# Optimization experiments

Measured on AMD Instinct MI355X. Metric: run time of the kernel, lower is better.

The kernel has to match this reference:

```python
import jax, jax.numpy as jnp
import numpy as np

TEMPERATURE = 0.07
EPS = 1e-8  # torch CosineSimilarity eps


def setup_inputs() -> dict:
    key = jax.random.key(0)
    k1, k2, k3 = jax.random.split(key, 3)
    N, D = 8192, 512
    features = jax.random.normal(k1, (N, D), dtype=jnp.float32)
    positive_mask = jax.random.randint(k2, (N, N), 0, 2, dtype=jnp.int32)
    negative_mask = jax.random.randint(k3, (N, N), 0, 2, dtype=jnp.int32)
    return {"features": features, "positive_mask": positive_mask, "negative_mask": negative_mask}


def reference(features, positive_mask, negative_mask):
    N = positive_mask.shape[0]
    self_contrast = 1.0 - jnp.eye(N, dtype=features.dtype)  # zero diagonal
    pos = positive_mask.astype(features.dtype) * self_contrast  # [N, N]
    neg = negative_mask.astype(features.dtype) * self_contrast  # [N, N]

    # cosine similarity via normalized matmul (same math as broadcasted CosineSimilarity)
    norm = jnp.maximum(jnp.linalg.norm(features, axis=1, keepdims=True), EPS)
    fn = features / norm  # [N, D]
    sim = jnp.matmul(fn, fn.T) / TEMPERATURE  # [N, N]

    logits_max = jax.lax.stop_gradient(jnp.max(sim, axis=1, keepdims=True))
    e = jnp.exp(sim - logits_max)  # [N, N]

    positives = e * pos
    log_neg_sum = jnp.log(jnp.sum(e * neg, axis=1, keepdims=True))  # [N, 1]
    log_prob = positives - log_neg_sum  # [N, N] (faithful to source: exp-masked, not log)

    cardinal = jnp.sum(pos, axis=1)
    cardinal = jnp.where(cardinal == 0, 1.0, cardinal)
    log_prob_sum = jnp.sum(log_prob * pos, axis=1)
    loss = -log_prob_sum / cardinal
    return jnp.mean(loss)
```

## Files before the change

kernel.cpp:

```cpp
#include <hip/hip_runtime.h>
#include <hip/hip_bf16.h>
#include <math.h>

#define NN 8192
#define DD 512
#define INV_T 14.285714285714286f
#define NWPR 128

typedef __attribute__((ext_vector_type(8))) short s16x8;
typedef __attribute__((ext_vector_type(4))) float f32x4;

__device__ __forceinline__ unsigned short f32_to_bf16(float f) {
  unsigned int u = __float_as_uint(f);
  u += 0x7FFFu + ((u >> 16) & 1u);
  return (unsigned short)(u >> 16);
}

__device__ __forceinline__ void async16(const void* g, void* l) {
  __builtin_amdgcn_global_load_lds((__attribute__((address_space(1))) void*)(void*)g,
                                   (__attribute__((address_space(3))) void*)l,
                                   16, 0, 0);
}

__global__ __launch_bounds__(256) void normalize_kernel(const float* __restrict__ f,
                                                        unsigned short* __restrict__ fnb) {
  const int wave = threadIdx.x >> 6;
  const int lane = threadIdx.x & 63;
  const int row  = blockIdx.x * 4 + wave;
  const float* src = f + (size_t)row * DD + lane * 8;
  float4 v0 = *(const float4*)src;
  float4 v1 = *(const float4*)(src + 4);
  float ss = v0.x*v0.x + v0.y*v0.y + v0.z*v0.z + v0.w*v0.w
           + v1.x*v1.x + v1.y*v1.y + v1.z*v1.z + v1.w*v1.w;
  #pragma unroll
  for (int o = 32; o; o >>= 1) ss += __shfl_xor(ss, o);
  const float r = 1.0f / fmaxf(sqrtf(ss), 1e-8f);
  ushort4 a, b;
  a.x = f32_to_bf16(v0.x * r); a.y = f32_to_bf16(v0.y * r);
  a.z = f32_to_bf16(v0.z * r); a.w = f32_to_bf16(v0.w * r);
  b.x = f32_to_bf16(v1.x * r); b.y = f32_to_bf16(v1.y * r);
  b.z = f32_to_bf16(v1.z * r); b.w = f32_to_bf16(v1.w * r);
  unsigned short* dst = fnb + (size_t)row * DD + lane * 8;
  *(ushort4*)dst = a;
  *(ushort4*)(dst + 4) = b;
}

__global__ __launch_bounds__(256) void pack_kernel(const int* __restrict__ posm,
                                                   const int* __restrict__ negm,
                                                   unsigned long long* __restrict__ pb,
                                                   unsigned long long* __restrict__ nb) {
  const int lane = threadIdx.x & 63;
  const long long gw = (long long)((blockIdx.x * 256 + threadIdx.x) >> 6);
  const long long nwaves = (long long)((gridDim.x * 256) >> 6);
  const long long NW = (long long)NN * NN / 64;
  for (long long w0 = gw * 8; w0 < NW; w0 += nwaves * 8) {
    unsigned long long bp[8], bn[8];
    #pragma unroll
    for (int u = 0; u < 8; ++u) {
      const size_t idx = (size_t)(w0 + u) * 64 + lane;
      const int p = __builtin_nontemporal_load(posm + idx);
      const int n = __builtin_nontemporal_load(negm + idx);
      bp[u] = __ballot(p != 0);
      bn[u] = __ballot(n != 0);
    }
    if (lane == 0) {
      #pragma unroll
      for (int u = 0; u < 8; u += 2) {
        ulonglong2 vp; vp.x = bp[u]; vp.y = bp[u + 1];
        ulonglong2 vn; vn.x = bn[u]; vn.y = bn[u + 1];
        *(ulonglong2*)(pb + w0 + u) = vp;
        *(ulonglong2*)(nb + w0 + u) = vn;
      }
    }
  }
}

__global__ __launch_bounds__(256) void fused_kernel(const unsigned short* __restrict__ fnb,
                                                    const unsigned long long* __restrict__ pb,
                                                    const unsigned long long* __restrict__ nb,
                                                    float* __restrict__ Spos,
                                                    float* __restrict__ Sneg,
                                                    float* __restrict__ Pcnt) {
  const int bid = blockIdx.x;
  int bi = (int)(64.5 - sqrt(64.5 * 64.5 - 2.0 * (double)bid));
  while (64 * bi - bi * (bi - 1) / 2 > bid) --bi;
  while (64 * (bi + 1) - (bi + 1) * bi / 2 <= bid) ++bi;
  const int bj = bi + (bid - (64 * bi - bi * (bi - 1) / 2));
  const int I = bi * 128;
  const int J = bj * 128;

  const int tid  = threadIdx.x;
  const int wave = tid >> 6;
  const int lane = tid & 63;
  const int wm = wave >> 1;
  const int wn = wave & 1;
  const int q   = lane >> 4;
  const int c16 = lane & 15;

  __shared__ alignas(16) unsigned short lA[128 * 32];
  __shared__ alignas(16) unsigned short lB[128 * 32];

  f32x4 acc[4][4];
  const f32x4 z4 = {0.f, 0.f, 0.f, 0.f};
  #pragma unroll
  for (int mt = 0; mt < 4; ++mt)
    #pragma unroll
    for (int nt = 0; nt < 4; ++nt) acc[mt][nt] = z4;

  for (int kk = 0; kk < DD / 32; ++kk) {
    const int k0 = kk * 32;
    #pragma unroll
    for (int c = 0; c < 2; ++c) {
      const int fidx = tid + c * 256;
      const int row  = fidx >> 2;
      const int p    = fidx & 3;
      const int csrc = (p ^ ((row >> 1) & 3)) & 3;
      async16(fnb + (size_t)(I + row) * DD + k0 + csrc * 8, (char*)lA + fidx * 16);
      async16(fnb + (size_t)(J + row) * DD + k0 + csrc * 8, (char*)lB + fidx * 16);
    }
    __syncthreads();

    s16x8 aF[4], bF[4];
    #pragma unroll
    for (int t = 0; t < 4; ++t) {
      const int arow = wm * 64 + t * 16 + c16;
      const int apos = (q ^ ((arow >> 1) & 3)) & 3;
      aF[t] = *(const s16x8*)((const char*)lA + arow * 64 + apos * 16);
      const int brow = wn * 64 + t * 16 + c16;
      const int bpos = (q ^ ((brow >> 1) & 3)) & 3;
      bF[t] = *(const s16x8*)((const char*)lB + brow * 64 + bpos * 16);
    }
    #pragma unroll
    for (int mt = 0; mt < 4; ++mt)
      #pragma unroll
      for (int nt = 0; nt < 4; ++nt)
        acc[mt][nt] = __builtin_amdgcn_mfma_f32_16x16x32_bf16(aF[mt], bF[nt], acc[mt][nt], 0, 0, 0);
    __syncthreads();
  }

  const bool offdiag = (bi != bj);
  const bool hasdiag = (bi == bj) && (wm == wn);
  const int jw = bj * 2 + wn;

  unsigned long long pT[4], nT[4];
  if (offdiag) {
    #pragma unroll
    for (int nt = 0; nt < 4; ++nt) {
      const int col = J + wn * 64 + nt * 16 + c16;
      const size_t tw = (size_t)col * NWPR + bi * 2 + wm;
      pT[nt] = pb[tw];
      nT[nt] = nb[tw];
    }
  }
  float tsp[4] = {0,0,0,0}, tsn[4] = {0,0,0,0};

  #pragma unroll
  for (int mt = 0; mt < 4; ++mt) {
    const int rbase = I + wm * 64 + mt * 16 + q * 4;
    unsigned long long pw[4], nw[4];
    #pragma unroll
    for (int r = 0; r < 4; ++r) {
      const size_t w = (size_t)(rbase + r) * NWPR + jw;
      pw[r] = pb[w];
      nw[r] = nb[w];
      if (hasdiag) {
        const unsigned long long m = ~(1ULL << (mt * 16 + q * 4 + r));
        pw[r] &= m;
        nw[r] &= m;
      }
    }
    float dsp[4] = {0,0,0,0}, dsn[4] = {0,0,0,0};
    #pragma unroll
    for (int nt = 0; nt < 4; ++nt) {
      float e[4];
      #pragma unroll
      for (int r = 0; r < 4; ++r)
        e[r] = __expf(acc[mt][nt][r] * INV_T - INV_T);
      const int bpos = nt * 16 + c16;
      #pragma unroll
      for (int r = 0; r < 4; ++r) {
        const float pf = (float)((pw[r] >> bpos) & 1ULL);
        const float nf = (float)((nw[r] >> bpos) & 1ULL);
        dsp[r] = fmaf(e[r], pf, dsp[r]);
        dsn[r] = fmaf(e[r], nf, dsn[r]);
      }
      if (offdiag) {
        const int bt = mt * 16 + q * 4;
        #pragma unroll
        for (int r = 0; r < 4; ++r) {
          tsp[nt] = fmaf(e[r], (float)((pT[nt] >> (bt + r)) & 1ULL), tsp[nt]);
          tsn[nt] = fmaf(e[r], (float)((nT[nt] >> (bt + r)) & 1ULL), tsn[nt]);
        }
      }
    }
    #pragma unroll
    for (int r = 0; r < 4; ++r) {
      float a = dsp[r], b = dsn[r];
      #pragma unroll
      for (int o = 1; o <= 8; o <<= 1) {
        a += __shfl_xor(a, o);
        b += __shfl_xor(b, o);
      }
      if (c16 == 0) {
        atomicAdd(&Spos[rbase + r], a);
        atomicAdd(&Sneg[rbase + r], b);
        atomicAdd(&Pcnt[rbase + r], (float)__popcll(pw[r]));
      }
    }
  }

  if (offdiag) {
    #pragma unroll
    for (int nt = 0; nt < 4; ++nt) {
      float a = tsp[nt], b = tsn[nt];
      a += __shfl_xor(a, 16); a += __shfl_xor(a, 32);
      b += __shfl_xor(b, 16); b += __shfl_xor(b, 32);
      if (q == 0) {
        const int col = J + wn * 64 + nt * 16 + c16;
        atomicAdd(&Spos[col], a);
        atomicAdd(&Sneg[col], b);
        atomicAdd(&Pcnt[col], (float)__popcll(pT[nt]));
      }
    }
  }
}

__global__ __launch_bounds__(256) void finalize_kernel(const float* __restrict__ Spos,
                                                       const float* __restrict__ Sneg,
                                                       const float* __restrict__ Pcnt,
                                                       float* __restrict__ out) {
  float local = 0.f;
  for (int i = threadIdx.x; i < NN; i += 256) {
    const float sp = Spos[i], sn = Sneg[i], pc = Pcnt[i];
    const float card = (pc == 0.f) ? 1.f : pc;
    local += (logf(sn) * pc - sp) / card;
  }
  #pragma unroll
  for (int o = 32; o; o >>= 1) local += __shfl_xor(local, o);
  __shared__ float red[4];
  if ((threadIdx.x & 63) == 0) red[threadIdx.x >> 6] = local;
  __syncthreads();
  if (threadIdx.x == 0)
    out[0] = (red[0] + red[1] + red[2] + red[3]) * (1.0f / (float)NN);
}

extern "C" void kernel_launch(void* const* d_in, const int* in_sizes, int n_in,
                              void* d_out, int out_size, void* d_ws, size_t ws_size,
                              hipStream_t stream) {
  const float* feat = (const float*)d_in[0];
  const int* posm   = (const int*)d_in[1];
  const int* negm   = (const int*)d_in[2];
  float* out = (float*)d_out;

  char* ws = (char*)d_ws;
  unsigned short* fnb = (unsigned short*)ws;
  unsigned long long* pbit = (unsigned long long*)(ws + (size_t)8 * 1024 * 1024);
  unsigned long long* nbit = (unsigned long long*)(ws + (size_t)16 * 1024 * 1024);
  float* Spos = (float*)(ws + (size_t)24 * 1024 * 1024);
  float* Sneg = Spos + NN;
  float* Pcnt = Sneg + NN;

  hipMemsetAsync(Spos, 0, 3 * NN * sizeof(float), stream);
  normalize_kernel<<<NN / 4, 256, 0, stream>>>(feat, fnb);
  pack_kernel<<<4096, 256, 0, stream>>>(posm, negm, pbit, nbit);
  fused_kernel<<<2080, 256, 0, stream>>>(fnb, pbit, nbit, Spos, Sneg, Pcnt);
  finalize_kernel<<<1, 256, 0, stream>>>(Spos, Sneg, Pcnt, out);
}
```

Measured before the change: 669.6 us.

## Fuse mask bit-packing into the fused GEMM kernel via LDS bitmasks

Removes the separate pack_kernel that turned the int32 masks into global bitmaps. Each block of the triangular GEMM now loads its own 128x128 tile of both masks, plus the transposed tile for off-diagonal blocks, ballots them into LDS bitmasks, and reads those in the epilogue. This avoids writing and re-reading the packed bitmaps and one kernel launch. The int32 mask traffic (512 MB total) is still read once. It now happens inside the GEMM kernel before the k-loop, which may serialize memory latency with compute unless occupancy hides it.

```diff
diff --git a/kernel.cpp b/kernel.cpp
--- a/kernel.cpp
+++ b/kernel.cpp
@@ -5,7 +5,6 @@
 #define NN 8192
 #define DD 512
 #define INV_T 14.285714285714286f
-#define NWPR 128
 
 typedef __attribute__((ext_vector_type(8))) short s16x8;
 typedef __attribute__((ext_vector_type(4))) float f32x4;
@@ -45,39 +44,9 @@
   *(ushort4*)(dst + 4) = b;
 }
 
-__global__ __launch_bounds__(256) void pack_kernel(const int* __restrict__ posm,
-                                                   const int* __restrict__ negm,
-                                                   unsigned long long* __restrict__ pb,
-                                                   unsigned long long* __restrict__ nb) {
-  const int lane = threadIdx.x & 63;
-  const long long gw = (long long)((blockIdx.x * 256 + threadIdx.x) >> 6);
-  const long long nwaves = (long long)((gridDim.x * 256) >> 6);
-  const long long NW = (long long)NN * NN / 64;
-  for (long long w0 = gw * 8; w0 < NW; w0 += nwaves * 8) {
-    unsigned long long bp[8], bn[8];
-    #pragma unroll
-    for (int u = 0; u < 8; ++u) {
-      const size_t idx = (size_t)(w0 + u) * 64 + lane;
-      const int p = __builtin_nontemporal_load(posm + idx);
-      const int n = __builtin_nontemporal_load(negm + idx);
-      bp[u] = __ballot(p != 0);
-      bn[u] = __ballot(n != 0);
-    }
-    if (lane == 0) {
-      #pragma unroll
-      for (int u = 0; u < 8; u += 2) {
-        ulonglong2 vp; vp.x = bp[u]; vp.y = bp[u + 1];
-        ulonglong2 vn; vn.x = bn[u]; vn.y = bn[u + 1];
-        *(ulonglong2*)(pb + w0 + u) = vp;
-        *(ulonglong2*)(nb + w0 + u) = vn;
-      }
-    }
-  }
-}
-
 __global__ __launch_bounds__(256) void fused_kernel(const unsigned short* __restrict__ fnb,
-                                                    const unsigned long long* __restrict__ pb,
-                                                    const unsigned long long* __restrict__ nb,
+                                                    const int* __restrict__ posm,
+                                                    const int* __restrict__ negm,
                                                     float* __restrict__ Spos,
                                                     float* __restrict__ Sneg,
                                                     float* __restrict__ Pcnt) {
@@ -88,6 +57,7 @@
   const int bj = bi + (bid - (64 * bi - bi * (bi - 1) / 2));
   const int I = bi * 128;
   const int J = bj * 128;
+  const bool offdiag = (bi != bj);
 
   const int tid  = threadIdx.x;
   const int wave = tid >> 6;
@@ -99,6 +69,36 @@
 
   __shared__ alignas(16) unsigned short lA[128 * 32];
   __shared__ alignas(16) unsigned short lB[128 * 32];
+  __shared__ alignas(16) unsigned long long mdir[2][128][2];
+  __shared__ alignas(16) unsigned long long mtr [2][128][2];
+
+  {
+    const int tile = wave >> 1;
+    const int msel = wave & 1;
+    const int R0 = tile ? J : I;
+    const int C0 = tile ? I : J;
+    const int* mb = msel ? negm : posm;
+    unsigned long long (*dst)[2] = tile ? mtr[msel] : mdir[msel];
+    if (!(tile && !offdiag)) {
+      for (int k = 0; k < 128; k += 8) {
+        int v[16];
+        #pragma unroll
+        for (int u = 0; u < 16; ++u)
+          v[u] = __builtin_nontemporal_load(
+              mb + (size_t)(R0 + k + (u >> 1)) * NN + C0 + (u & 1) * 64 + lane);
+        unsigned long long b[16];
+        #pragma unroll
+        for (int u = 0; u < 16; ++u) b[u] = __ballot(v[u] != 0);
+        if (lane == 0) {
+          #pragma unroll
+          for (int u = 0; u < 16; u += 2) {
+            ulonglong2 t; t.x = b[u]; t.y = b[u + 1];
+            *(ulonglong2*)&dst[k + (u >> 1)][0] = t;
+          }
+        }
+      }
+    }
+  }
 
   f32x4 acc[4][4];
   const f32x4 z4 = {0.f, 0.f, 0.f, 0.f};
@@ -138,31 +138,28 @@
     __syncthreads();
   }
 
-  const bool offdiag = (bi != bj);
   const bool hasdiag = (bi == bj) && (wm == wn);
-  const int jw = bj * 2 + wn;
 
   unsigned long long pT[4], nT[4];
   if (offdiag) {
     #pragma unroll
     for (int nt = 0; nt < 4; ++nt) {
-      const int col = J + wn * 64 + nt * 16 + c16;
-      const size_t tw = (size_t)col * NWPR + bi * 2 + wm;
-      pT[nt] = pb[tw];
-      nT[nt] = nb[tw];
+      const int cl = wn * 64 + nt * 16 + c16;
+      pT[nt] = mtr[0][cl][wm];
+      nT[nt] = mtr[1][cl][wm];
     }
   }
   float tsp[4] = {0,0,0,0}, tsn[4] = {0,0,0,0};
 
   #pragma unroll
   for (int mt = 0; mt < 4; ++mt) {
-    const int rbase = I + wm * 64 + mt * 16 + q * 4;
+    const int rl = wm * 64 + mt * 16 + q * 4;
+    const int rbase = I + rl;
     unsigned long long pw[4], nw[4];
     #pragma unroll
     for (int r = 0; r < 4; ++r) {
-      const size_t w = (size_t)(rbase + r) * NWPR + jw;
-      pw[r] = pb[w];
-      nw[r] = nb[w];
+      pw[r] = mdir[0][rl + r][wn];
+      nw[r] = mdir[1][rl + r][wn];
       if (hasdiag) {
         const unsigned long long m = ~(1ULL << (mt * 16 + q * 4 + r));
         pw[r] &= m;
@@ -254,15 +251,12 @@
 
   char* ws = (char*)d_ws;
   unsigned short* fnb = (unsigned short*)ws;
-  unsigned long long* pbit = (unsigned long long*)(ws + (size_t)8 * 1024 * 1024);
-  unsigned long long* nbit = (unsigned long long*)(ws + (size_t)16 * 1024 * 1024);
-  float* Spos = (float*)(ws + (size_t)24 * 1024 * 1024);
+  float* Spos = (float*)(ws + (size_t)8 * 1024 * 1024);
   float* Sneg = Spos + NN;
   float* Pcnt = Sneg + NN;
 
   hipMemsetAsync(Spos, 0, 3 * NN * sizeof(float), stream);
   normalize_kernel<<<NN / 4, 256, 0, stream>>>(feat, fnb);
-  pack_kernel<<<4096, 256, 0, stream>>>(posm, negm, pbit, nbit);
-  fused_kernel<<<2080, 256, 0, stream>>>(fnb, pbit, nbit, Spos, Sneg, Pcnt);
+  fused_kernel<<<2080, 256, 0, stream>>>(fnb, posm, negm, Spos, Sneg, Pcnt);
   finalize_kernel<<<1, 256, 0, stream>>>(Spos, Sneg, Pcnt, out);
 }
```

New measurement: 654.4 us. -2.3%, faster.

## Vectorize mask packing with prefetch and reduce tile partials in shared memory

Applied to the files above, without the earlier changes.

The pack kernel now loads 16-byte vectors per lane with a double-buffered prefetch across 8 iterations. It writes the bitmasks in a permuted bit order that matches the MFMA accumulator layout, so the fused kernel extracts bits with simpler shifts. The fused kernel applies exp to all accumulators up front and reduces row and column partial sums in shared memory before issuing one set of global atomics per tile, which cuts global atomic traffic. It also sets a launch bound of 3 blocks per SM. The bit-order permutation must stay consistent between producer and consumer, and the new occupancy bound risks register pressure.

```diff
diff --git a/kernel.cpp b/kernel.cpp
--- a/kernel.cpp
+++ b/kernel.cpp
@@ -5,10 +5,10 @@
 #define NN 8192
 #define DD 512
 #define INV_T 14.285714285714286f
-#define NWPR 128
 
 typedef __attribute__((ext_vector_type(8))) short s16x8;
 typedef __attribute__((ext_vector_type(4))) float f32x4;
+typedef __attribute__((ext_vector_type(4))) int   i32x4;
 
 __device__ __forceinline__ unsigned short f32_to_bf16(float f) {
   unsigned int u = __float_as_uint(f);
@@ -50,37 +50,68 @@
                                                    unsigned long long* __restrict__ pb,
                                                    unsigned long long* __restrict__ nb) {
   const int lane = threadIdx.x & 63;
-  const long long gw = (long long)((blockIdx.x * 256 + threadIdx.x) >> 6);
-  const long long nwaves = (long long)((gridDim.x * 256) >> 6);
-  const long long NW = (long long)NN * NN / 64;
-  for (long long w0 = gw * 8; w0 < NW; w0 += nwaves * 8) {
-    unsigned long long bp[8], bn[8];
-    #pragma unroll
-    for (int u = 0; u < 8; ++u) {
-      const size_t idx = (size_t)(w0 + u) * 64 + lane;
-      const int p = __builtin_nontemporal_load(posm + idx);
-      const int n = __builtin_nontemporal_load(negm + idx);
-      bp[u] = __ballot(p != 0);
-      bn[u] = __ballot(n != 0);
-    }
-    if (lane == 0) {
-      #pragma unroll
-      for (int u = 0; u < 8; u += 2) {
-        ulonglong2 vp; vp.x = bp[u]; vp.y = bp[u + 1];
-        ulonglong2 vn; vn.x = bn[u]; vn.y = bn[u + 1];
-        *(ulonglong2*)(pb + w0 + u) = vp;
-        *(ulonglong2*)(nb + w0 + u) = vn;
-      }
-    }
-  }
-}
-
-__global__ __launch_bounds__(256) void fused_kernel(const unsigned short* __restrict__ fnb,
-                                                    const unsigned long long* __restrict__ pb,
-                                                    const unsigned long long* __restrict__ nb,
-                                                    float* __restrict__ Spos,
-                                                    float* __restrict__ Sneg,
-                                                    float* __restrict__ Pcnt) {
+  const int gw = (int)((blockIdx.x * 256 + threadIdx.x) >> 6);
+  const int lofs = lane * 4;
+
+  i32x4 vp[2][4], vn[2][4];
+  #pragma unroll
+  for (int u = 0; u < 4; ++u) {
+    const size_t b = ((size_t)gw * 4 + u) * 256 + lofs;
+    vp[0][u] = __builtin_nontemporal_load((const i32x4*)(posm + b));
+    vn[0][u] = __builtin_nontemporal_load((const i32x4*)(negm + b));
+  }
+  #pragma unroll 1
+  for (int it = 0; it < 8; ++it) {
+    const int cur = it & 1, nxt = cur ^ 1;
+    if (it < 7) {
+      #pragma unroll
+      for (int u = 0; u < 4; ++u) {
+        const size_t b = (((size_t)(it + 1) * 8192 + gw) * 4 + u) * 256 + lofs;
+        vp[nxt][u] = __builtin_nontemporal_load((const i32x4*)(posm + b));
+        vn[nxt][u] = __builtin_nontemporal_load((const i32x4*)(negm + b));
+      }
+    }
+    const long long s0 = ((long long)it * 8192 + gw) * 4;
+    #pragma unroll
+    for (int u = 0; u < 4; ++u) {
+      {
+        const i32x4 v = vp[cur][u];
+        const unsigned long long bx = __ballot(v.x != 0), by = __ballot(v.y != 0),
+                                 bz = __ballot(v.z != 0), bw = __ballot(v.w != 0);
+        if (lane < 2) {
+          const int k0 = lane * 2;
+          ulonglong2 t;
+          t.x = ((bx >> (16*k0)) & 0xFFFFull)        | (((by >> (16*k0)) & 0xFFFFull) << 16)
+              | (((bz >> (16*k0)) & 0xFFFFull) << 32) | (((bw >> (16*k0)) & 0xFFFFull) << 48);
+          t.y = ((bx >> (16*k0+16)) & 0xFFFFull)        | (((by >> (16*k0+16)) & 0xFFFFull) << 16)
+              | (((bz >> (16*k0+16)) & 0xFFFFull) << 32) | (((bw >> (16*k0+16)) & 0xFFFFull) << 48);
+          *(ulonglong2*)(pb + (s0 + u) * 4 + k0) = t;
+        }
+      }
+      {
+        const i32x4 v = vn[cur][u];
+        const unsigned long long bx = __ballot(v.x != 0), by = __ballot(v.y != 0),
+                                 bz = __ballot(v.z != 0), bw = __ballot(v.w != 0);
+        if (lane < 2) {
+          const int k0 = lane * 2;
+          ulonglong2 t;
+          t.x = ((bx >> (16*k0)) & 0xFFFFull)        | (((by >> (16*k0)) & 0xFFFFull) << 16)
+              | (((bz >> (16*k0)) & 0xFFFFull) << 32) | (((bw >> (16*k0)) & 0xFFFFull) << 48);
+          t.y = ((bx >> (16*k0+16)) & 0xFFFFull)        | (((by >> (16*k0+16)) & 0xFFFFull) << 16)
+              | (((bz >> (16*k0+16)) & 0xFFFFull) << 32) | (((bw >> (16*k0+16)) & 0xFFFFull) << 48);
+          *(ulonglong2*)(nb + (s0 + u) * 4 + k0) = t;
+        }
+      }
+    }
+  }
+}
+
+__global__ __launch_bounds__(256, 3) void fused_kernel(const unsigned short* __restrict__ fnb,
+                                                       const unsigned long long* __restrict__ pb,
+                                                       const unsigned long long* __restrict__ nb,
+                                                       float* __restrict__ Spos,
+                                                       float* __restrict__ Sneg,
+                                                       float* __restrict__ Pcnt) {
   const int bid = blockIdx.x;
   int bi = (int)(64.5 - sqrt(64.5 * 64.5 - 2.0 * (double)bid));
   while (64 * bi - bi * (bi - 1) / 2 > bid) --bi;
@@ -88,6 +119,7 @@
   const int bj = bi + (bid - (64 * bi - bi * (bi - 1) / 2));
   const int I = bi * 128;
   const int J = bj * 128;
+  const bool offdiag = (bi != bj);
 
   const int tid  = threadIdx.x;
   const int wave = tid >> 6;
@@ -99,6 +131,8 @@
 
   __shared__ alignas(16) unsigned short lA[128 * 32];
   __shared__ alignas(16) unsigned short lB[128 * 32];
+  __shared__ float sacc[2][128][3];
+  for (int t = tid; t < 2 * 128 * 3; t += 256) ((float*)sacc)[t] = 0.f;
 
   f32x4 acc[4][4];
   const f32x4 z4 = {0.f, 0.f, 0.f, 0.f};
@@ -138,90 +172,102 @@
     __syncthreads();
   }
 
-  const bool offdiag = (bi != bj);
   const bool hasdiag = (bi == bj) && (wm == wn);
-  const int jw = bj * 2 + wn;
-
-  unsigned long long pT[4], nT[4];
+
+  unsigned long long dpw[4][4], dnw[4][4];
+  #pragma unroll
+  for (int mt = 0; mt < 4; ++mt)
+    #pragma unroll
+    for (int r = 0; r < 4; ++r) {
+      const size_t a = (size_t)(I + wm * 64 + mt * 16 + q * 4 + r) * 128 + bj * 2 + wn;
+      dpw[mt][r] = pb[a];
+      dnw[mt][r] = nb[a];
+    }
+  unsigned long long tpw[4], tnw[4];
   if (offdiag) {
     #pragma unroll
     for (int nt = 0; nt < 4; ++nt) {
-      const int col = J + wn * 64 + nt * 16 + c16;
-      const size_t tw = (size_t)col * NWPR + bi * 2 + wm;
-      pT[nt] = pb[tw];
-      nT[nt] = nb[tw];
-    }
-  }
-  float tsp[4] = {0,0,0,0}, tsn[4] = {0,0,0,0};
-
+      const size_t a = (size_t)(J + wn * 64 + nt * 16 + c16) * 128 + bi * 2 + wm;
+      tpw[nt] = pb[a];
+      tnw[nt] = nb[a];
+    }
+  }
+
+  #pragma unroll
+  for (int mt = 0; mt < 4; ++mt)
+    #pragma unroll
+    for (int nt = 0; nt < 4; ++nt)
+      #pragma unroll
+      for (int r = 0; r < 4; ++r)
+        acc[mt][nt][r] = __expf(acc[mt][nt][r] * INV_T - INV_T);
+
+  const int shd = (c16 >> 2) + (c16 & 3) * 16;
   #pragma unroll
   for (int mt = 0; mt < 4; ++mt) {
-    const int rbase = I + wm * 64 + mt * 16 + q * 4;
-    unsigned long long pw[4], nw[4];
+    const int rl = wm * 64 + mt * 16 + q * 4;
     #pragma unroll
     for (int r = 0; r < 4; ++r) {
-      const size_t w = (size_t)(rbase + r) * NWPR + jw;
-      pw[r] = pb[w];
-      nw[r] = nb[w];
+      unsigned long long wp = dpw[mt][r], wnn = dnw[mt][r];
       if (hasdiag) {
-        const unsigned long long m = ~(1ULL << (mt * 16 + q * 4 + r));
-        pw[r] &= m;
-        nw[r] &= m;
-      }
-    }
-    float dsp[4] = {0,0,0,0}, dsn[4] = {0,0,0,0};
+        const unsigned long long m = ~(1ULL << (mt * 4 + q + 16 * r));
+        wp &= m; wnn &= m;
+      }
+      float dsp = 0.f, dsn = 0.f;
+      #pragma unroll
+      for (int nt = 0; nt < 4; ++nt) {
+        const float e = acc[mt][nt][r];
+        dsp = fmaf(e, (float)((wp  >> (nt * 4 + shd)) & 1ULL), dsp);
+        dsn = fmaf(e, (float)((wnn >> (nt * 4 + shd)) & 1ULL), dsn);
+      }
+      #pragma unroll
+      for (int o = 1; o <= 8; o <<= 1) {
+        dsp += __shfl_xor(dsp, o);
+        dsn += __shfl_xor(dsn, o);
+      }
+      if (c16 == 0) {
+        atomicAdd(&sacc[0][rl + r][0], dsp);
+        atomicAdd(&sacc[0][rl + r][1], dsn);
+        atomicAdd(&sacc[0][rl + r][2], (float)__popcll(wp));
+      }
+    }
+  }
+
+  if (offdiag) {
     #pragma unroll
     for (int nt = 0; nt < 4; ++nt) {
-      float e[4];
-      #pragma unroll
-      for (int r = 0; r < 4; ++r)
-        e[r] = __expf(acc[mt][nt][r] * INV_T - INV_T);
-      const int bpos = nt * 16 + c16;
-      #pragma unroll
-      for (int r = 0; r < 4; ++r) {
-        const float pf = (float)((pw[r] >> bpos) & 1ULL);
-        const float nf = (float)((nw[r] >> bpos) & 1ULL);
-        dsp[r] = fmaf(e[r], pf, dsp[r]);
-        dsn[r] = fmaf(e[r], nf, dsn[r]);
-      }
-      if (offdiag) {
-        const int bt = mt * 16 + q * 4;
+      const int cl = wn * 64 + nt * 16 + c16;
+      float ts = 0.f, tn = 0.f;
+      #pragma unroll
+      for (int mt = 0; mt < 4; ++mt) {
+        const int sh = mt * 4 + q;
         #pragma unroll
         for (int r = 0; r < 4; ++r) {
-          tsp[nt] = fmaf(e[r], (float)((pT[nt] >> (bt + r)) & 1ULL), tsp[nt]);
-          tsn[nt] = fmaf(e[r], (float)((nT[nt] >> (bt + r)) & 1ULL), tsn[nt]);
+          const float e = acc[mt][nt][r];
+          ts = fmaf(e, (float)((tpw[nt] >> (sh + 16 * r)) & 1ULL), ts);
+          tn = fmaf(e, (float)((tnw[nt] >> (sh + 16 * r)) & 1ULL), tn);
         }
       }
-    }
-    #pragma unroll
-    for (int r = 0; r < 4; ++r) {
-      float a = dsp[r], b = dsn[r];
-      #pragma unroll
-      for (int o = 1; o <= 8; o <<= 1) {
-        a += __shfl_xor(a, o);
-        b += __shfl_xor(b, o);
-      }
-      if (c16 == 0) {
-        atomicAdd(&Spos[rbase + r], a);
-        atomicAdd(&Sneg[rbase + r], b);
-        atomicAdd(&Pcnt[rbase + r], (float)__popcll(pw[r]));
-      }
-    }
-  }
-
-  if (offdiag) {
-    #pragma unroll
-    for (int nt = 0; nt < 4; ++nt) {
-      float a = tsp[nt], b = tsn[nt];
-      a += __shfl_xor(a, 16); a += __shfl_xor(a, 32);
-      b += __shfl_xor(b, 16); b += __shfl_xor(b, 32);
+      ts += __shfl_xor(ts, 16); ts += __shfl_xor(ts, 32);
+      tn += __shfl_xor(tn, 16); tn += __shfl_xor(tn, 32);
       if (q == 0) {
-        const int col = J + wn * 64 + nt * 16 + c16;
-        atomicAdd(&Spos[col], a);
-        atomicAdd(&Sneg[col], b);
-        atomicAdd(&Pcnt[col], (float)__popcll(pT[nt]));
-      }
-    }
+        atomicAdd(&sacc[1][cl][0], ts);
+        atomicAdd(&sacc[1][cl][1], tn);
+        atomicAdd(&sacc[1][cl][2], (float)__popcll(tpw[nt]));
+      }
+    }
+  }
+
+  __syncthreads();
+
+  const int r = tid & 127;
+  if (tid < 128) {
+    atomicAdd(&Spos[I + r], sacc[0][r][0]);
+    atomicAdd(&Sneg[I + r], sacc[0][r][1]);
+    atomicAdd(&Pcnt[I + r], sacc[0][r][2]);
+  } else if (offdiag) {
+    atomicAdd(&Spos[J + r], sacc[1][r][0]);
+    atomicAdd(&Sneg[J + r], sacc[1][r][1]);
+    atomicAdd(&Pcnt[J + r], sacc[1][r][2]);
   }
 }
 
@@ -262,7 +308,7 @@
 
   hipMemsetAsync(Spos, 0, 3 * NN * sizeof(float), stream);
   normalize_kernel<<<NN / 4, 256, 0, stream>>>(feat, fnb);
-  pack_kernel<<<4096, 256, 0, stream>>>(posm, negm, pbit, nbit);
+  pack_kernel<<<2048, 256, 0, stream>>>(posm, negm, pbit, nbit);
   fused_kernel<<<2080, 256, 0, stream>>>(fnb, pbit, nbit, Spos, Sneg, Pcnt);
   finalize_kernel<<<1, 256, 0, stream>>>(Spos, Sneg, Pcnt, out);
 }
```

New measurement: 643.8 us. 3.9% less time.
